# Optimization experiments

Hardware: AMD Instinct MI355X
Metric: run time of the kernel (lower is better)

## Reference

```python
import jax, jax.numpy as jnp
import numpy as np

DT = 1.0
EPS = 1e-6


def setup_inputs() -> dict:
    key = jax.random.key(0)
    k1, k2, k3, k4 = jax.random.split(key, 4)
    batch, in_ch, out_ch, state_dim, T = 16, 256, 256, 256, 8192
    u = jax.random.normal(k1, (batch, in_ch, T), dtype=jnp.float32)
    raw_lambda = jax.random.normal(k2, (state_dim,), dtype=jnp.float32)
    B_c = jax.random.normal(k3, (in_ch, state_dim), dtype=jnp.float32) * (1.0 / in_ch ** 0.5)
    C = jax.random.normal(k4, (state_dim, out_ch), dtype=jnp.float32) * (1.0 / state_dim ** 0.5)
    return {"u": u, "raw_lambda": raw_lambda, "B_c": B_c, "C": C}


def reference(u, raw_lambda, B_c, C):
    # ZOH discretization of diagonal SSM (all-real here since raw_lambda is real)
    lam = -jax.nn.softplus(raw_lambda)                 # (N,)
    A_d = jnp.exp(lam * DT)                            # (N,)
    factor = jnp.where(jnp.abs(lam) > EPS, (A_d - 1.0) / lam, jnp.full_like(lam, DT))
    B_d = B_c * factor[None, :]                        # (in_ch, N)

    # Precompute driving inputs for every step in one big GEMM: (T, B, N)
    x = jnp.einsum('bct,cn->tbn', u, B_d)

    batch, state_dim = u.shape[0], raw_lambda.shape[0]

    def step(s, x_t):
        s = s * A_d[None, :] + x_t                     # diagonal recurrence
        return s, s

    s0 = jnp.zeros((batch, state_dim), dtype=u.dtype)
    _, states = jax.lax.scan(step, s0, x)              # states: (T, B, N)

    # Project all states at once: y (B, out_ch, T)
    y = jnp.einsum('tbn,no->bot', states, C)
    return y
```

## Files before the change

kernel.cpp:

```cpp
#include <hip/hip_runtime.h>
#include <math.h>

typedef __attribute__((ext_vector_type(8)))  short short8;
typedef __attribute__((ext_vector_type(16))) float f32x16;

#define B_  16
#define C_  256
#define N_  256
#define O_  256
#define T_  8192
#define L_  64
#define NC_ 128

#define GLL16(gptr, lptr) \
  __builtin_amdgcn_global_load_lds((const __attribute__((address_space(1))) void*)(gptr), \
                                   (__attribute__((address_space(3))) void*)(lptr), 16, 0, 0)

__device__ inline unsigned short f2bf(float x) {
    unsigned u = __float_as_uint(x);
    u += 0x7fff + ((u >> 16) & 1);
    return (unsigned short)(u >> 16);
}
__device__ inline float bf2f(unsigned short h) {
    return __uint_as_float(((unsigned)h) << 16);
}
__device__ inline f32x16 zero16() {
    f32x16 z;
    #pragma unroll
    for (int i = 0; i < 16; ++i) z[i] = 0.f;
    return z;
}

__global__ __launch_bounds__(256) void k_prep(
    const float* __restrict__ raw_lambda, const float* __restrict__ B_c,
    const float* __restrict__ Cmat,
    float* __restrict__ Ad, float* __restrict__ AL,
    unsigned short* __restrict__ BdKf, unsigned short* __restrict__ CKf)
{
    const int r = blockIdx.x;
    const int t = threadIdx.x;
    const int kk = r >> 5, ri = r & 31;
    const int s = ri >> 4, hi = (ri >> 3) & 1, j = ri & 7;
    const int nt = t >> 5, l = (hi << 5) | (t & 31);
    const int idx = (((kk * 8 + nt) * 2 + s) * 64 + l) * 8 + j;

    if (blockIdx.y == 0) {
        const float x  = raw_lambda[t];
        const float sp = (x > 20.f) ? x : log1pf(expf(x));
        const float lam = -sp;
        const float ad  = expf(lam);
        const float factor = (fabsf(lam) > 1e-6f) ? (ad - 1.f) / lam : 1.f;
        if (r == 0) {
            Ad[t] = ad;
            float al = ad;
            #pragma unroll
            for (int i = 0; i < 6; ++i) al *= al;
            AL[t] = al;
        }
        BdKf[idx] = f2bf(B_c[r * N_ + t] * factor);
    } else {
        CKf[idx] = f2bf(Cmat[r * O_ + t]);
    }
}

__global__ __launch_bounds__(256) void k_phaseA(
    const float* __restrict__ u, const unsigned short* __restrict__ BdKf,
    const float* __restrict__ Ad, float* __restrict__ p_last,
    unsigned short* __restrict__ X, int doX)
{
    __shared__ __align__(16) unsigned short ut[2][2688];
    __shared__ __align__(16) unsigned short bb[2][8192];

    const int k = blockIdx.x, b = blockIdx.y;
    const int tid = threadIdx.x;
    const int w = tid >> 6, l = tid & 63, lo = l & 31, hi = l >> 5;
    const int t0 = k * L_;
    const float* ub = u + (size_t)b * C_ * T_ + t0;

    const float adq0 = Ad[(2 * w + 0) * 32 + lo];
    const float adq1 = Ad[(2 * w + 1) * 32 + lo];

    auto load_u = [&](float4 v[2], int kk) {
        #pragma unroll
        for (int q = 0; q < 2; ++q) {
            const int i = q * 256 + tid, cl = i >> 4, t4 = i & 15;
            v[q] = *(const float4*)(ub + (size_t)(kk * 32 + cl) * T_ + t4 * 4);
        }
    };
    auto cvt_ut = [&](const float4 v[2], unsigned short* utb) {
        unsigned* ud = (unsigned*)utb;
        #pragma unroll
        for (int q = 0; q < 2; ++q) {
            const int i = q * 256 + tid, cl = i >> 4, t4 = i & 15;
            float4 a = v[q], p;
            p.x = __shfl_xor(a.x, 16); p.y = __shfl_xor(a.y, 16);
            p.z = __shfl_xor(a.z, 16); p.w = __shfl_xor(a.w, 16);
            const bool odd = (cl & 1) != 0;
            const float l0 = odd ? p.z : a.x, h0 = odd ? a.z : p.x;
            const float l1 = odd ? p.w : a.y, h1 = odd ? a.w : p.y;
            const int r0 = odd ? 2 : 0;
            ud[(4 * t4 + r0    ) * 21 + (cl >> 1)] = f2bf(l0) | ((unsigned)f2bf(h0) << 16);
            ud[(4 * t4 + r0 + 1) * 21 + (cl >> 1)] = f2bf(l1) | ((unsigned)f2bf(h1) << 16);
        }
    };
    auto stage_bb = [&](int kk, int buf) {
        const char* src = (const char*)(BdKf + kk * 8192);
        #pragma unroll
        for (int q = 0; q < 4; ++q)
            GLL16(src + q * 4096 + w * 1024 + (l << 4),
                  (char*)bb[buf] + q * 4096 + w * 1024);
    };

    f32x16 a00 = zero16(), a01 = zero16(), a10 = zero16(), a11 = zero16();
    float4 va[2], vb[2];

    load_u(va, 0);
    stage_bb(0, 0);
    cvt_ut(va, ut[0]);
    load_u(va, 1);
    __syncthreads();

    #pragma unroll
    for (int kk = 0; kk < 8; ++kk) {
        const int cur = kk & 1;
        if (kk < 7) stage_bb(kk + 1, cur ^ 1);
        if (kk < 6) { if (kk & 1) load_u(va, kk + 2); else load_u(vb, kk + 2); }
        #pragma unroll
        for (int s = 0; s < 2; ++s) {
            const short8 fa0 = *(const short8*)(ut[cur] + (lo     ) * 42 + s * 16 + hi * 8);
            const short8 fa1 = *(const short8*)(ut[cur] + (32 + lo) * 42 + s * 16 + hi * 8);
            const short8 fb0 = *(const short8*)(bb[cur] + (((2 * w + 0) * 2 + s) * 64 + l) * 8);
            const short8 fb1 = *(const short8*)(bb[cur] + (((2 * w + 1) * 2 + s) * 64 + l) * 8);
            a00 = __builtin_amdgcn_mfma_f32_32x32x16_bf16(fa0, fb0, a00, 0, 0, 0);
            a01 = __builtin_amdgcn_mfma_f32_32x32x16_bf16(fa0, fb1, a01, 0, 0, 0);
            a10 = __builtin_amdgcn_mfma_f32_32x32x16_bf16(fa1, fb0, a10, 0, 0, 0);
            a11 = __builtin_amdgcn_mfma_f32_32x32x16_bf16(fa1, fb1, a11, 0, 0, 0);
        }
        if (kk < 7) { if (kk & 1) cvt_ut(vb, ut[cur ^ 1]); else cvt_ut(va, ut[cur ^ 1]); }
        __syncthreads();
    }

    if (doX) {
        unsigned* Xd = (unsigned*)X + (size_t)(k * B_ + b) * 8192;
        #pragma unroll
        for (int f = 0; f < 4; ++f) {
            const f32x16 a = (f == 0) ? a00 : (f == 1) ? a01 : (f == 2) ? a10 : a11;
            unsigned dw[8];
            #pragma unroll
            for (int d = 0; d < 8; ++d)
                dw[d] = f2bf(a[2 * d]) | ((unsigned)f2bf(a[2 * d + 1]) << 16);
            unsigned* base = Xd + w * 2048 + f * 512 + l * 4;
            *(int4*)(base)       = *(const int4*)&dw[0];
            *(int4*)(base + 256) = *(const int4*)&dw[4];
        }
    }

    {
        float p[2];
        #pragma unroll
        for (int q = 0; q < 2; ++q) {
            const float ad = q ? adq1 : adq0;
            const float ad2 = ad * ad, ad4 = ad2 * ad2, ad8 = ad4 * ad4;
            const float ad16 = ad8 * ad8, ad32 = ad16 * ad16;
            float full[2];
            #pragma unroll
            for (int tt = 0; tt < 2; ++tt) {
                const f32x16 a = (tt == 0) ? (q == 0 ? a00 : a01)
                                           : (q == 0 ? a10 : a11);
                float v[4];
                #pragma unroll
                for (int g = 0; g < 4; ++g)
                    v[g] = fmaf(fmaf(fmaf(a[4*g], ad, a[4*g+1]), ad, a[4*g+2]), ad, a[4*g+3]);
                const float H = fmaf(fmaf(fmaf(v[0], ad8, v[1]), ad8, v[2]), ad8, v[3]);
                float P = hi ? H : H * ad4;
                P += __shfl_xor(P, 32);
                full[tt] = P;
            }
            p[q] = fmaf(full[0], ad32, full[1]);
        }
        if (hi == 0) {
            float* dst = p_last + (size_t)(k * B_ + b) * N_;
            dst[(2 * w + 0) * 32 + lo] = p[0];
            dst[(2 * w + 1) * 32 + lo] = p[1];
        }
    }
}

__global__ __launch_bounds__(256) void k_phaseB(
    const float* __restrict__ p_last, const float* __restrict__ AL,
    float* __restrict__ carry)
{
    __shared__ float buf[32 * 256];
    const int b = blockIdx.x, n = threadIdx.x;
    const float al = AL[n];
    float cur = 0.f;
    for (int kc = 0; kc < 4; ++kc) {
        __syncthreads();
        #pragma unroll
        for (int q = 0; q < 32; ++q)
            buf[q * 256 + n] = p_last[((size_t)(kc * 32 + q) * B_ + b) * N_ + n];
        __syncthreads();
        #pragma unroll
        for (int q = 0; q < 32; ++q) {
            carry[((size_t)(kc * 32 + q) * B_ + b) * N_ + n] = cur;
            cur = fmaf(cur, al, buf[q * 256 + n]);
        }
    }
}

__global__ __launch_bounds__(256) void k_phaseC(
    const unsigned short* __restrict__ X, const unsigned short* __restrict__ CKf,
    const float* __restrict__ Ad, const float* __restrict__ carry,
    float* __restrict__ y)
{
    __shared__ __align__(16) unsigned short xs[16896];
    __shared__ __align__(16) unsigned short bb[2][8192];

    const int k = blockIdx.x, b = blockIdx.y;
    const int tid = threadIdx.x;
    const int w = tid >> 6, l = tid & 63, lo = l & 31, hi = l >> 5;
    const int t0 = k * L_;

    auto stage_bb = [&](int kk, int buf) {
        const char* src = (const char*)(CKf + kk * 8192);
        #pragma unroll
        for (int q = 0; q < 4; ++q)
            GLL16(src + q * 4096 + w * 1024 + (l << 4),
                  (char*)bb[buf] + q * 4096 + w * 1024);
    };

    stage_bb(0, 0);
    {
        const char* src = (const char*)X + (size_t)(k * B_ + b) * 32768;
        #pragma unroll
        for (int q = 0; q < 8; ++q)
            GLL16(src + q * 4096 + w * 1024 + (l << 4),
                  (char*)xs + q * 4096 + w * 1024);
    }
    const float cv = carry[(size_t)(k * B_ + b) * N_ + tid];
    const float ad = Ad[tid];
    __syncthreads();

    unsigned arr[2][2][8];
    {
        const unsigned* xd = (const unsigned*)xs;
        const int w2 = tid >> 6, q2 = (tid >> 5) & 1, lo2 = tid & 31;
        #pragma unroll
        for (int tt = 0; tt < 2; ++tt)
            #pragma unroll
            for (int h2 = 0; h2 < 2; ++h2) {
                const unsigned* p = xd + w2 * 2048 + (tt * 2 + q2) * 512
                                       + (h2 * 32 + lo2) * 4;
                *(int4*)&arr[tt][h2][0] = *(const int4*)(p);
                *(int4*)&arr[tt][h2][4] = *(const int4*)(p + 256);
            }
    }
    __syncthreads();

    {
        const int nb = tid >> 3, nl = tid & 7;
        float s = cv;
        #pragma unroll
        for (int tt = 0; tt < 2; ++tt)
            #pragma unroll
            for (int g = 0; g < 4; ++g)
                #pragma unroll
                for (int h2 = 0; h2 < 2; ++h2) {
                    const unsigned d0 = arr[tt][h2][2 * g];
                    const unsigned d1 = arr[tt][h2][2 * g + 1];
                    const int tb = tt * 32 + 8 * g + 4 * h2;
                    const int swz = (((nb ^ ((tb >> 3) & 3)) << 3) | nl);
                    s = fmaf(s, ad, bf2f((unsigned short)(d0 & 0xffff)));
                    xs[(tb + 0) * 264 + swz] = f2bf(s);
                    s = fmaf(s, ad, bf2f((unsigned short)(d0 >> 16)));
                    xs[(tb + 1) * 264 + swz] = f2bf(s);
                    s = fmaf(s, ad, bf2f((unsigned short)(d1 & 0xffff)));
                    xs[(tb + 2) * 264 + swz] = f2bf(s);
                    s = fmaf(s, ad, bf2f((unsigned short)(d1 >> 16)));
                    xs[(tb + 3) * 264 + swz] = f2bf(s);
                }
    }
    __syncthreads();

    f32x16 c00 = zero16(), c01 = zero16(), c10 = zero16(), c11 = zero16();
    #pragma unroll
    for (int kk = 0; kk < 8; ++kk) {
        const int cur = kk & 1;
        if (kk < 7) stage_bb(kk + 1, cur ^ 1);
        #pragma unroll
        for (int s = 0; s < 2; ++s) {
            short8 fa[2];
            #pragma unroll
            for (int tt = 0; tt < 2; ++tt) {
                const int t = tt * 32 + lo;
                const int blk = (kk * 4 + s * 2 + hi) ^ ((t >> 3) & 3);
                fa[tt] = *(const short8*)(xs + t * 264 + blk * 8);
            }
            const short8 fb0 = *(const short8*)(bb[cur] + (((2 * w + 0) * 2 + s) * 64 + l) * 8);
            const short8 fb1 = *(const short8*)(bb[cur] + (((2 * w + 1) * 2 + s) * 64 + l) * 8);
            c00 = __builtin_amdgcn_mfma_f32_32x32x16_bf16(fa[0], fb0, c00, 0, 0, 0);
            c01 = __builtin_amdgcn_mfma_f32_32x32x16_bf16(fa[0], fb1, c01, 0, 0, 0);
            c10 = __builtin_amdgcn_mfma_f32_32x32x16_bf16(fa[1], fb0, c10, 0, 0, 0);
            c11 = __builtin_amdgcn_mfma_f32_32x32x16_bf16(fa[1], fb1, c11, 0, 0, 0);
        }
        __syncthreads();
    }

    #pragma unroll
    for (int tt = 0; tt < 2; ++tt)
        #pragma unroll
        for (int q = 0; q < 2; ++q) {
            const f32x16 a = (tt == 0) ? (q == 0 ? c00 : c01) : (q == 0 ? c10 : c11);
            const int o = (2 * w + q) * 32 + lo;
            float* yo = y + ((size_t)b * O_ + o) * T_ + t0 + tt * 32 + hi * 4;
            #pragma unroll
            for (int g = 0; g < 4; ++g) {
                float4 v;
                v.x = a[g * 4 + 0]; v.y = a[g * 4 + 1];
                v.z = a[g * 4 + 2]; v.w = a[g * 4 + 3];
                *(float4*)(yo + g * 8) = v;
            }
        }
}

__device__ __forceinline__ void gemm1_rc(
    const float* __restrict__ u, const unsigned short* __restrict__ BdKf,
    int b, int k, unsigned short* xs, unsigned short* ut, unsigned short* bb)
{
    const int tid = threadIdx.x;
    const int w = tid >> 6, l = tid & 63, lo = l & 31, hi = l >> 5;
    const int t0 = k * L_;
    f32x16 a00 = zero16(), a01 = zero16(), a10 = zero16(), a11 = zero16();
    for (int kk = 0; kk < 8; ++kk) {
        #pragma unroll
        for (int q = 0; q < 2; ++q) {
            const int i = q * 256 + tid, cl = i >> 4, t4 = i & 15;
            const float4 v = *(const float4*)(
                u + ((size_t)b * C_ + kk * 32 + cl) * T_ + t0 + t4 * 4);
            ut[(t4 * 4 + 0) * 40 + cl] = f2bf(v.x);
            ut[(t4 * 4 + 1) * 40 + cl] = f2bf(v.y);
            ut[(t4 * 4 + 2) * 40 + cl] = f2bf(v.z);
            ut[(t4 * 4 + 3) * 40 + cl] = f2bf(v.w);
        }
        {
            const unsigned short* src = BdKf + kk * 8192;
            #pragma unroll
            for (int q = 0; q < 4; ++q) {
                const int i16 = q * 256 + tid;
                *(int4*)(bb + i16 * 8) = *(const int4*)(src + i16 * 8);
            }
        }
        __syncthreads();
        #pragma unroll
        for (int s = 0; s < 2; ++s) {
            const short8 fa0 = *(const short8*)(ut + (0 * 32 + lo) * 40 + s * 16 + hi * 8);
            const short8 fa1 = *(const short8*)(ut + (1 * 32 + lo) * 40 + s * 16 + hi * 8);
            const short8 fb0 = *(const short8*)(bb + (((2 * w + 0) * 2 + s) * 64 + l) * 8);
            const short8 fb1 = *(const short8*)(bb + (((2 * w + 1) * 2 + s) * 64 + l) * 8);
            a00 = __builtin_amdgcn_mfma_f32_32x32x16_bf16(fa0, fb0, a00, 0, 0, 0);
            a01 = __builtin_amdgcn_mfma_f32_32x32x16_bf16(fa0, fb1, a01, 0, 0, 0);
            a10 = __builtin_amdgcn_mfma_f32_32x32x16_bf16(fa1, fb0, a10, 0, 0, 0);
            a11 = __builtin_amdgcn_mfma_f32_32x32x16_bf16(fa1, fb1, a11, 0, 0, 0);
        }
        __syncthreads();
    }
    #pragma unroll
    for (int tt = 0; tt < 2; ++tt)
        #pragma unroll
        for (int q = 0; q < 2; ++q) {
            const f32x16 a = (tt == 0) ? (q == 0 ? a00 : a01) : (q == 0 ? a10 : a11);
            const int n = (2 * w + q) * 32 + lo;
            #pragma unroll
            for (int g = 0; g < 4; ++g)
                #pragma unroll
                for (int p = 0; p < 2; ++p)
                    *(unsigned*)(xs + n * 66 + tt * 32 + hi * 4 + g * 8 + p * 2)
                        = f2bf(a[g * 4 + 2 * p]) | ((unsigned)f2bf(a[g * 4 + 2 * p + 1]) << 16);
        }
    __syncthreads();
}

__global__ __launch_bounds__(256) void k_phaseC_rc(
    const float* __restrict__ u, const unsigned short* __restrict__ BdKf,
    const unsigned short* __restrict__ CKf, const float* __restrict__ Ad,
    const float* __restrict__ carry, float* __restrict__ y)
{
    __shared__ __align__(16) unsigned short xs[16896];
    __shared__ __align__(16) unsigned short ut[2560];
    __shared__ __align__(16) unsigned short bb[8192];

    const int k = blockIdx.x, b = blockIdx.y;
    const int tid = threadIdx.x;
    const int w = tid >> 6, l = tid & 63, lo = l & 31, hi = l >> 5;
    const int t0 = k * L_;

    gemm1_rc(u, BdKf, b, k, xs, ut, bb);

    {
        const float a = Ad[tid];
        float s = carry[((size_t)k * B_ + b) * N_ + tid];
        float st[64];
        #pragma unroll
        for (int m = 0; m < 32; ++m) {
            const unsigned dw = *(const unsigned*)(xs + tid * 66 + 2 * m);
            s = fmaf(s, a, bf2f((unsigned short)(dw & 0xffff)));  st[2 * m] = s;
            s = fmaf(s, a, bf2f((unsigned short)(dw >> 16)));     st[2 * m + 1] = s;
        }
        __syncthreads();
        #pragma unroll
        for (int t = 0; t < 64; ++t) xs[t * 264 + tid] = f2bf(st[t]);
    }
    __syncthreads();

    f32x16 c00 = zero16(), c01 = zero16(), c10 = zero16(), c11 = zero16();
    for (int kk = 0; kk < 8; ++kk) {
        __syncthreads();
        {
            const unsigned short* src = CKf + kk * 8192;
            #pragma unroll
            for (int q = 0; q < 4; ++q) {
                const int i16 = q * 256 + tid;
                *(int4*)(bb + i16 * 8) = *(const int4*)(src + i16 * 8);
            }
        }
        __syncthreads();
        #pragma unroll
        for (int s = 0; s < 2; ++s) {
            const short8 fa0 = *(const short8*)(xs + (0 * 32 + lo) * 264 + kk * 32 + s * 16 + hi * 8);
            const short8 fa1 = *(const short8*)(xs + (1 * 32 + lo) * 264 + kk * 32 + s * 16 + hi * 8);
            const short8 fb0 = *(const short8*)(bb + (((2 * w + 0) * 2 + s) * 64 + l) * 8);
            const short8 fb1 = *(const short8*)(bb + (((2 * w + 1) * 2 + s) * 64 + l) * 8);
            c00 = __builtin_amdgcn_mfma_f32_32x32x16_bf16(fa0, fb0, c00, 0, 0, 0);
            c01 = __builtin_amdgcn_mfma_f32_32x32x16_bf16(fa0, fb1, c01, 0, 0, 0);
            c10 = __builtin_amdgcn_mfma_f32_32x32x16_bf16(fa1, fb0, c10, 0, 0, 0);
            c11 = __builtin_amdgcn_mfma_f32_32x32x16_bf16(fa1, fb1, c11, 0, 0, 0);
        }
    }

    #pragma unroll
    for (int tt = 0; tt < 2; ++tt)
        #pragma unroll
        for (int q = 0; q < 2; ++q) {
            const f32x16 a = (tt == 0) ? (q == 0 ? c00 : c01) : (q == 0 ? c10 : c11);
            const int o = (2 * w + q) * 32 + lo;
            float* yo = y + ((size_t)b * O_ + o) * T_ + t0 + tt * 32 + hi * 4;
            #pragma unroll
            for (int g = 0; g < 4; ++g) {
                float4 v;
                v.x = a[g * 4 + 0]; v.y = a[g * 4 + 1];
                v.z = a[g * 4 + 2]; v.w = a[g * 4 + 3];
                *(float4*)(yo + g * 8) = v;
            }
        }
}

extern "C" void kernel_launch(void* const* d_in, const int* in_sizes, int n_in,
                              void* d_out, int out_size, void* d_ws, size_t ws_size,
                              hipStream_t stream)
{
    const float* u  = (const float*)d_in[0];
    const float* rl = (const float*)d_in[1];
    const float* Bc = (const float*)d_in[2];
    const float* Cm = (const float*)d_in[3];
    float* y  = (float*)d_out;
    char*  ws = (char*)d_ws;

    float* Ad     = (float*)(ws + 0);
    float* AL     = (float*)(ws + 1024);
    float* p_last = (float*)(ws + 2048);
    float* carry  = (float*)(ws + 2048 + 2097152);
    unsigned short* BdKf = (unsigned short*)(ws + 2048 + 2 * 2097152);
    unsigned short* CKf  = (unsigned short*)(ws + 2048 + 2 * 2097152 + 131072);
    unsigned short* X    = (unsigned short*)(ws + 2048 + 2 * 2097152 + 2 * 131072);
    const size_t need = 2048 + 2ull * 2097152 + 2ull * 131072
                      + (size_t)NC_ * B_ * 32768;
    const int doX = (ws_size >= need) ? 1 : 0;

    k_prep  <<<dim3(256, 2),  dim3(256), 0, stream>>>(rl, Bc, Cm, Ad, AL, BdKf, CKf);
    k_phaseA<<<dim3(NC_, B_), dim3(256), 0, stream>>>(u, BdKf, Ad, p_last, X, doX);
    k_phaseB<<<dim3(B_),      dim3(256), 0, stream>>>(p_last, AL, carry);
    if (doX)
        k_phaseC<<<dim3(NC_, B_), dim3(256), 0, stream>>>(X, CKf, Ad, carry, y);
    else
        k_phaseC_rc<<<dim3(NC_, B_), dim3(256), 0, stream>>>(u, BdKf, CKf, Ad, carry, y);
}
```

Measured before the change: 120.0 us.

## Load whole u tile up front into swizzled LDS instead of pipelined chunks

Phase A now issues all 16 float4 loads of the 256-channel by 64-timestep u tile at once and converts the whole tile to bf16 into a single LDS buffer with an XOR swizzle. The per-k-step double-buffered u loading and conversion inside the MFMA loop is removed. The aim is to get more global loads in flight and drop the interleaved conversion work from the main loop. In exchange it uses more registers and LDS (about 33KB for u plus 32KB for the B buffers), which may lower occupancy, and the u load latency is no longer overlapped with MFMA work.

After: 122.6 us. 1.02x slower.

```diff
diff --git a/kernel.cpp b/kernel.cpp
--- a/kernel.cpp
+++ b/kernel.cpp
@@ -68,7 +68,7 @@
     const float* __restrict__ Ad, float* __restrict__ p_last,
     unsigned short* __restrict__ X, int doX)
 {
-    __shared__ __align__(16) unsigned short ut[2][2688];
+    __shared__ __align__(16) unsigned short ut[16896];
     __shared__ __align__(16) unsigned short bb[2][8192];
 
     const int k = blockIdx.x, b = blockIdx.y;
@@ -80,17 +80,26 @@
     const float adq0 = Ad[(2 * w + 0) * 32 + lo];
     const float adq1 = Ad[(2 * w + 1) * 32 + lo];
 
-    auto load_u = [&](float4 v[2], int kk) {
-        #pragma unroll
-        for (int q = 0; q < 2; ++q) {
-            const int i = q * 256 + tid, cl = i >> 4, t4 = i & 15;
-            v[q] = *(const float4*)(ub + (size_t)(kk * 32 + cl) * T_ + t4 * 4);
-        }
+    auto stage_bb = [&](int kk, int buf) {
+        const char* src = (const char*)(BdKf + kk * 8192);
+        #pragma unroll
+        for (int q = 0; q < 4; ++q)
+            GLL16(src + q * 4096 + w * 1024 + (l << 4),
+                  (char*)bb[buf] + q * 4096 + w * 1024);
     };
-    auto cvt_ut = [&](const float4 v[2], unsigned short* utb) {
-        unsigned* ud = (unsigned*)utb;
-        #pragma unroll
-        for (int q = 0; q < 2; ++q) {
+
+    stage_bb(0, 0);
+
+    float4 v[16];
+    #pragma unroll
+    for (int q = 0; q < 16; ++q) {
+        const int i = q * 256 + tid, cl = i >> 4, t4 = i & 15;
+        v[q] = *(const float4*)(ub + (size_t)cl * T_ + t4 * 4);
+    }
+    {
+        unsigned* ud = (unsigned*)ut;
+        #pragma unroll
+        for (int q = 0; q < 16; ++q) {
             const int i = q * 256 + tid, cl = i >> 4, t4 = i & 15;
             float4 a = v[q], p;
             p.x = __shfl_xor(a.x, 16); p.y = __shfl_xor(a.y, 16);
@@ -99,36 +108,30 @@
             const float l0 = odd ? p.z : a.x, h0 = odd ? a.z : p.x;
             const float l1 = odd ? p.w : a.y, h1 = odd ? a.w : p.y;
             const int r0 = odd ? 2 : 0;
-            ud[(4 * t4 + r0    ) * 21 + (cl >> 1)] = f2bf(l0) | ((unsigned)f2bf(h0) << 16);
-            ud[(4 * t4 + r0 + 1) * 21 + (cl >> 1)] = f2bf(l1) | ((unsigned)f2bf(h1) << 16);
-        }
-    };
-    auto stage_bb = [&](int kk, int buf) {
-        const char* src = (const char*)(BdKf + kk * 8192);
-        #pragma unroll
-        for (int q = 0; q < 4; ++q)
-            GLL16(src + q * 4096 + w * 1024 + (l << 4),
-                  (char*)bb[buf] + q * 4096 + w * 1024);
-    };
+            const int nb = cl >> 3, jd = (cl >> 1) & 3;
+            const int tA = 4 * t4 + r0, tB = tA + 1;
+            const int xsw = (tA >> 3) & 3;
+            ud[tA * 132 + (((nb ^ xsw) << 2) | jd)] =
+                f2bf(l0) | ((unsigned)f2bf(h0) << 16);
+            ud[tB * 132 + (((nb ^ xsw) << 2) | jd)] =
+                f2bf(l1) | ((unsigned)f2bf(h1) << 16);
+        }
+    }
+    __syncthreads();
 
     f32x16 a00 = zero16(), a01 = zero16(), a10 = zero16(), a11 = zero16();
-    float4 va[2], vb[2];
-
-    load_u(va, 0);
-    stage_bb(0, 0);
-    cvt_ut(va, ut[0]);
-    load_u(va, 1);
-    __syncthreads();
-
     #pragma unroll
     for (int kk = 0; kk < 8; ++kk) {
         const int cur = kk & 1;
         if (kk < 7) stage_bb(kk + 1, cur ^ 1);
-        if (kk < 6) { if (kk & 1) load_u(va, kk + 2); else load_u(vb, kk + 2); }
         #pragma unroll
         for (int s = 0; s < 2; ++s) {
-            const short8 fa0 = *(const short8*)(ut[cur] + (lo     ) * 42 + s * 16 + hi * 8);
-            const short8 fa1 = *(const short8*)(ut[cur] + (32 + lo) * 42 + s * 16 + hi * 8);
+            const int blk8 = kk * 4 + s * 2 + hi;
+            short8 fa0, fa1;
+            { const int t = lo;
+              fa0 = *(const short8*)(ut + t * 264 + ((blk8 ^ ((t >> 3) & 3)) << 3)); }
+            { const int t = 32 + lo;
+              fa1 = *(const short8*)(ut + t * 264 + ((blk8 ^ ((t >> 3) & 3)) << 3)); }
             const short8 fb0 = *(const short8*)(bb[cur] + (((2 * w + 0) * 2 + s) * 64 + l) * 8);
             const short8 fb1 = *(const short8*)(bb[cur] + (((2 * w + 1) * 2 + s) * 64 + l) * 8);
             a00 = __builtin_amdgcn_mfma_f32_32x32x16_bf16(fa0, fb0, a00, 0, 0, 0);
@@ -136,7 +139,6 @@
             a10 = __builtin_amdgcn_mfma_f32_32x32x16_bf16(fa1, fb0, a10, 0, 0, 0);
             a11 = __builtin_amdgcn_mfma_f32_32x32x16_bf16(fa1, fb1, a11, 0, 0, 0);
         }
-        if (kk < 7) { if (kk & 1) cvt_ut(vb, ut[cur ^ 1]); else cvt_ut(va, ut[cur ^ 1]); }
         __syncthreads();
     }
 
@@ -167,11 +169,11 @@
             for (int tt = 0; tt < 2; ++tt) {
                 const f32x16 a = (tt == 0) ? (q == 0 ? a00 : a01)
                                            : (q == 0 ? a10 : a11);
-                float v[4];
+                float v2[4];
                 #pragma unroll
                 for (int g = 0; g < 4; ++g)
-                    v[g] = fmaf(fmaf(fmaf(a[4*g], ad, a[4*g+1]), ad, a[4*g+2]), ad, a[4*g+3]);
-                const float H = fmaf(fmaf(fmaf(v[0], ad8, v[1]), ad8, v[2]), ad8, v[3]);
+                    v2[g] = fmaf(fmaf(fmaf(a[4*g], ad, a[4*g+1]), ad, a[4*g+2]), ad, a[4*g+3]);
+                const float H = fmaf(fmaf(fmaf(v2[0], ad8, v2[1]), ad8, v2[2]), ad8, v2[3]);
                 float P = hi ? H : H * ad4;
                 P += __shfl_xor(P, 32);
                 full[tt] = P;
```
